# Kernel tuning notes

Measured on AMD Instinct MI355X. Metric: run time of the kernel, lower is better.

Reference implementation:

```python
import jax, jax.numpy as jnp
import numpy as np

# --- config (matches init_kwargs) ---
B, L = 16, 1024            # batch, max_seq_len
S = L - 1                  # effective sequence length
D = 768                    # attention_dim
H = 8                      # n_heads
DH = D // 3 * 2            # per-head Q/K/V out dim = 512
HID = 256                  # hidden_dim (EntireEmbedding output)
FF = 3072                  # ffnn_dim
N_A = 10000                # n_assessments = offsets[0]
N_CATE, N_CONT = 4, 6
EPS = 1e-5


def setup_inputs() -> dict:
    key = jax.random.key(0)
    ks = jax.random.split(key, 24)
    f = lambda k, shp, s=0.02: (jax.random.normal(k, shp, dtype=jnp.float32) * s)
    inp = {
        "cate_x": jax.random.randint(ks[0], (B, L, N_CATE), 0, N_A),
        "cont_x": jax.random.normal(ks[1], (B, L, N_CONT), dtype=jnp.float32),
        "mask": jax.random.randint(ks[2], (B, L), 0, 2),
        "targets": jax.random.randint(ks[3], (B, L), 0, 2),
        # embeddings (padding_idx=0 rows zeroed)
        "M_emb": f(ks[4], ((N_A + 1) * 2 - 1, D)).at[0].set(0.0),
        "E_emb": f(ks[5], (N_A + 1, D)).at[0].set(0.0),
        "pos_emb": f(ks[6], (S, D)),
        # EntireEmbedding stand-in: cate embedding + linear over cont feats -> HID
        "cate_emb": f(ks[7], (N_A + 1, HID)).at[0].set(0.0),
        "cont_W": f(ks[8], (N_CONT, HID)),
        "cont_b": jnp.zeros((HID,), jnp.float32),
        # per-head Q/K/V, stacked over head axis
        "WQ": f(ks[9], (H, D, DH)),
        "bQ": jnp.zeros((H, DH), jnp.float32),
        "WK": f(ks[10], (H, D + HID, DH)),
        "bK": jnp.zeros((H, DH), jnp.float32),
        "WV": f(ks[11], (H, D + HID, DH)),
        "bV": jnp.zeros((H, DH), jnp.float32),
        "W0": f(ks[12], (H * DH, D)),
        "ln_g": jnp.ones((D,), jnp.float32),
        "ln_b": jnp.zeros((D,), jnp.float32),
        "ffn_W1": f(ks[13], (D, FF)),
        "ffn_b1": jnp.zeros((FF,), jnp.float32),
        "ffn_W2": f(ks[14], (FF, D)),
        "ffn_b2": jnp.zeros((D,), jnp.float32),
        # FinalConnecting stand-in: Linear(D, 1)
        "fin_W": f(ks[15], (D, 1)),
        "fin_b": jnp.zeros((1,), jnp.float32),
    }
    return inp


def reference(cate_x, cont_x, mask, targets, M_emb, E_emb, pos_emb, cate_emb,
              cont_W, cont_b, WQ, bQ, WK, bK, WV, bV, W0, ln_g, ln_b,
              ffn_W1, ffn_b1, ffn_W2, ffn_b2, fin_W, fin_b):
    # additive mask, faithful to the original (triu over [B,S]!)
    new_mask = jnp.triu(jnp.ones((B, S), jnp.float32), k=-1) * 100000.0 - 100000.0

    assessments = cate_x[:, :-1, 0]                 # [B,S]
    interactions = targets[:, :-1]
    y = assessments + interactions * N_A            # interaction ids
    next_assessments = cate_x[:, 1:, 0]

    M_hat = M_emb[y] + pos_emb[None]                # [B,S,D]
    comb = cate_emb[cate_x[..., 0]] + cont_x @ cont_W + cont_b   # [B,L,HID]
    E_hat = jnp.concatenate([E_emb[next_assessments], comb[:, 1:, :]], axis=-1)  # [B,S,D+HID]

    # all heads at once (faithful per-head Q/K/V linears, stacked)
    Q = jnp.einsum('bsd,hde->hbse', M_hat, WQ) + bQ[:, None, None, :]
    K = jnp.einsum('bsd,hde->hbse', E_hat, WK) + bK[:, None, None, :]
    V = jnp.einsum('bsd,hde->hbse', E_hat, WV) + bV[:, None, None, :]

    score = jnp.einsum('hbqe,hbke->hbqk', Q, K) / jnp.sqrt(jnp.asarray(DH, Q.dtype))
    score = score + new_mask[None, :, None, :]      # broadcast over query axis
    attn = jax.nn.softmax(score, axis=-1)
    Z = jnp.einsum('hbqk,hbke->hbqe', attn, V)      # [H,B,S,DH]
    Zc = jnp.transpose(Z, (1, 2, 0, 3)).reshape(B, S, H * DH)  # head-major concat

    z = Zc @ W0                                     # [B,S,D]
    fz = jax.nn.relu(z @ ffn_W1 + ffn_b1) @ ffn_W2 + ffn_b2  # dropout off (eval)
    h = z + fz
    mu = jnp.mean(h, axis=-1, keepdims=True)
    var = jnp.mean((h - mu) ** 2, axis=-1, keepdims=True)
    zn = (h - mu) / jnp.sqrt(var + EPS) * ln_g + ln_b

    out = (zn @ fin_W + fin_b)[..., 0]              # [B,S]
    return out
```

## Files before the change

kernel.cpp:

```cpp
#include <hip/hip_runtime.h>
#include <hip/hip_bf16.h>

constexpr int B_   = 16;
constexpr int L_   = 1024;
constexpr int S_   = 1023;
constexpr int D_   = 768;
constexpr int H_   = 8;
constexpr int DH_  = 512;
constexpr int HID_ = 256;
constexpr int FF_  = 3072;
constexpr int NA_  = 10000;
constexpr int NCATE_ = 4;
constexpr int NCONT_ = 6;
constexpr float EPS_ = 1e-5f;
constexpr long BSR_ = (long)B_ * S_;
constexpr int SLD_ = 1024;

constexpr long COMB_SZ = BSR_ * HID_;
constexpr long IDX_PAD = 49152;
constexpr long QKV_SZ  = BSR_ * DH_;
constexpr long SC_SZ   = (long)B_ * S_ * SLD_;
constexpr long ZO_SZ   = BSR_ * D_;
constexpr size_t WS_NEED_BYTES =
    (size_t)(COMB_SZ + IDX_PAD + 3 * QKV_SZ + SC_SZ + ZO_SZ) * 4;

__device__ __forceinline__ float blk_reduce_sum(float v, float* sm) {
#pragma unroll
    for (int off = 32; off > 0; off >>= 1) v += __shfl_down(v, off, 64);
    const int lane = threadIdx.x & 63, wv = threadIdx.x >> 6;
    if (lane == 0) sm[wv] = v;
    __syncthreads();
    float t = (threadIdx.x < 4) ? sm[threadIdx.x] : 0.f;
    t += __shfl_down(t, 2, 64);
    t += __shfl_down(t, 1, 64);
    if (threadIdx.x == 0) sm[4] = t;
    __syncthreads();
    float r = sm[4];
    __syncthreads();
    return r;
}

__device__ __forceinline__ float blk_reduce_max(float v, float* sm) {
#pragma unroll
    for (int off = 32; off > 0; off >>= 1) v = fmaxf(v, __shfl_down(v, off, 64));
    const int lane = threadIdx.x & 63, wv = threadIdx.x >> 6;
    if (lane == 0) sm[wv] = v;
    __syncthreads();
    float t = (threadIdx.x < 4) ? sm[threadIdx.x] : -3.4e38f;
    t = fmaxf(t, __shfl_down(t, 2, 64));
    t = fmaxf(t, __shfl_down(t, 1, 64));
    if (threadIdx.x == 0) sm[4] = t;
    __syncthreads();
    float r = sm[4];
    __syncthreads();
    return r;
}

__global__ __launch_bounds__(256) void sentinel_k(float* __restrict__ out, int n)
{
    const int i = blockIdx.x * 256 + threadIdx.x;
    if (i < n) out[i] = 1e30f;
}

__global__ __launch_bounds__(256) void prep_k(
    const int* __restrict__ cate_x, const float* __restrict__ cont_x,
    const int* __restrict__ targets,
    const float* __restrict__ cate_emb, const float* __restrict__ cont_W,
    const float* __restrict__ cont_b,
    int* __restrict__ yArr, int* __restrict__ nxArr, int* __restrict__ sArr,
    float* __restrict__ comb)
{
    const int row = blockIdx.x;
    const int b = row / S_;
    const int s = row - b * S_;
    const int nx = cate_x[((long)b * L_ + s + 1) * NCATE_];
    if (threadIdx.x == 0) {
        yArr[row]  = cate_x[((long)b * L_ + s) * NCATE_] + targets[(long)b * L_ + s] * NA_;
        nxArr[row] = nx;
        sArr[row]  = s;
    }
    const float* cx = cont_x + ((long)b * L_ + s + 1) * NCONT_;
    float cv[NCONT_];
#pragma unroll
    for (int i = 0; i < NCONT_; ++i) cv[i] = cx[i];
    const int j = threadIdx.x;
    float acc = cont_b[j];
#pragma unroll
    for (int i = 0; i < NCONT_; ++i) acc = fmaf(cv[i], cont_W[i * HID_ + j], acc);
    comb[(long)row * HID_ + j] = cate_emb[(long)nx * HID_ + j] + acc;
}

template<int TSZ, int AMODE, bool TB, bool BIAS, bool RELU, bool ADDC, bool ACCUM, bool KVF>
__global__ __launch_bounds__(256) void sgemm_k(
    const float* __restrict__ A, const float* __restrict__ A2,
    const int* __restrict__ rIdx, const int* __restrict__ rS,
    const float* __restrict__ Bm, const float* __restrict__ Bm2,
    const float* __restrict__ bias, const float* __restrict__ bias2,
    const float* __restrict__ Cadd, float* __restrict__ C, float* __restrict__ C2,
    int M, int N, int Kd, int lda, int ldb, int ldc,
    long sA, long sB, long sC, float alpha)
{
    constexpr int BK = 16;
    constexpr int TM = TSZ / 16;
    constexpr int NL = TSZ / 64;
    constexpr int NF4M = TSZ / 4 - 1;
    constexpr int SHB  = (TSZ == 128) ? 5 : 4;
    __shared__ float As[BK][TSZ];
    __shared__ float Bs[BK][TSZ];

    const int tid = threadIdx.x;
    const int tx = tid & 15;
    const int ty = tid >> 4;
    const int rowBase = blockIdx.y * TSZ;
    int colBase = blockIdx.x * TSZ;
    const int bz = blockIdx.z;

    if constexpr (KVF) {
        if (colBase >= DH_) {
            Bm = Bm2;
            if constexpr (BIAS) bias = bias2;
            C = C2;
            colBase -= DH_;
        }
    }
    if constexpr (AMODE == 0) A += (long)bz * sA;
    Bm += (long)bz * sB;
    C += (long)bz * sC;
    if constexpr (ADDC) Cadd += (long)bz * sC;

    float acc[TM][TM];
#pragma unroll
    for (int i = 0; i < TM; ++i)
#pragma unroll
        for (int j = 0; j < TM; ++j) acc[i][j] = 0.f;

    for (int k0 = 0; k0 < Kd; k0 += BK) {
#pragma unroll
        for (int u = 0; u < NL; ++u) {
            const int f = tid + u * 256;
            const int r = f >> 2;
            const int k4 = (f & 3) * 4;
            const int gk = k0 + k4;
            float v0 = 0.f, v1 = 0.f, v2 = 0.f, v3 = 0.f;
            const int gr = rowBase + r;
            if (gr < M) {
                if constexpr (AMODE == 0) {
                    const float* p = A + (long)gr * lda + gk;
                    if (gk + 3 < Kd) {
                        float4 v = *(const float4*)p;
                        v0 = v.x; v1 = v.y; v2 = v.z; v3 = v.w;
                    } else {
                        if (gk + 0 < Kd) v0 = p[0];
                        if (gk + 1 < Kd) v1 = p[1];
                        if (gk + 2 < Kd) v2 = p[2];
                    }
                } else if constexpr (AMODE == 1) {
                    const int y = rIdx[gr];
                    const int s = rS[gr];
                    const float4 a = *(const float4*)(A  + (long)y * D_ + gk);
                    const float4 p = *(const float4*)(A2 + (long)s * D_ + gk);
                    v0 = a.x + p.x; v1 = a.y + p.y; v2 = a.z + p.z; v3 = a.w + p.w;
                } else {
                    if (gk < D_) {
                        const int nx = rIdx[gr];
                        const float4 a = *(const float4*)(A + (long)nx * D_ + gk);
                        v0 = a.x; v1 = a.y; v2 = a.z; v3 = a.w;
                    } else {
                        const float4 a = *(const float4*)(A2 + (long)gr * HID_ + (gk - D_));
                        v0 = a.x; v1 = a.y; v2 = a.z; v3 = a.w;
                    }
                }
            }
            As[k4 + 0][r] = v0; As[k4 + 1][r] = v1;
            As[k4 + 2][r] = v2; As[k4 + 3][r] = v3;
        }
        if constexpr (!TB) {
#pragma unroll
            for (int u = 0; u < NL; ++u) {
                const int f = tid + u * 256;
                const int kk = f >> SHB;
                const int n4 = (f & NF4M) * 4;
                const int gk = k0 + kk;
                const int gc = colBase + n4;
                float v0 = 0.f, v1 = 0.f, v2 = 0.f, v3 = 0.f;
                if (gk < Kd) {
                    const float* p = Bm + (long)gk * ldb + gc;
                    if (gc + 3 < N) {
                        float4 v = *(const float4*)p;
                        v0 = v.x; v1 = v.y; v2 = v.z; v3 = v.w;
                    } else {
                        if (gc + 0 < N) v0 = p[0];
                        if (gc + 1 < N) v1 = p[1];
                        if (gc + 2 < N) v2 = p[2];
                        if (gc + 3 < N) v3 = p[3];
                    }
                }
                Bs[kk][n4 + 0] = v0; Bs[kk][n4 + 1] = v1;
                Bs[kk][n4 + 2] = v2; Bs[kk][n4 + 3] = v3;
            }
        } else {
#pragma unroll
            for (int u = 0; u < NL; ++u) {
                const int f = tid + u * 256;
                const int n = f >> 2;
                const int k4 = (f & 3) * 4;
                float v0 = 0.f, v1 = 0.f, v2 = 0.f, v3 = 0.f;
                const int gn = colBase + n;
                if (gn < N) {
                    const float* p = Bm + (long)gn * ldb + k0 + k4;
                    if (k0 + k4 + 3 < Kd) {
                        float4 v = *(const float4*)p;
                        v0 = v.x; v1 = v.y; v2 = v.z; v3 = v.w;
                    } else {
                        if (k0 + k4 + 0 < Kd) v0 = p[0];
                        if (k0 + k4 + 1 < Kd) v1 = p[1];
                        if (k0 + k4 + 2 < Kd) v2 = p[2];
                        if (k0 + k4 + 3 < Kd) v3 = p[3];
                    }
                }
                Bs[k4 + 0][n] = v0; Bs[k4 + 1][n] = v1;
                Bs[k4 + 2][n] = v2; Bs[k4 + 3][n] = v3;
            }
        }
        __syncthreads();

#pragma unroll
        for (int kk = 0; kk < BK; ++kk) {
            float a[TM], b[TM];
#pragma unroll
            for (int ih = 0; ih < TM / 4; ++ih) {
                *(float4*)&a[ih * 4] = *(const float4*)&As[kk][ih * 64 + ty * 4];
                *(float4*)&b[ih * 4] = *(const float4*)&Bs[kk][ih * 64 + tx * 4];
            }
#pragma unroll
            for (int i = 0; i < TM; ++i)
#pragma unroll
                for (int j = 0; j < TM; ++j)
                    acc[i][j] = fmaf(a[i], b[j], acc[i][j]);
        }
        __syncthreads();
    }

#pragma unroll
    for (int i = 0; i < TM; ++i) {
        const int r = rowBase + (i >> 2) * 64 + ty * 4 + (i & 3);
        if (r >= M) continue;
#pragma unroll
        for (int j = 0; j < TM; ++j) {
            const int c = colBase + (j >> 2) * 64 + tx * 4 + (j & 3);
            if (c >= N) continue;
            float v = acc[i][j] * alpha;
            if constexpr (BIAS) v += bias[c];
            if constexpr (ADDC) v += Cadd[(long)r * ldc + c];
            if constexpr (RELU) v = fmaxf(v, 0.f);
            const long idx = (long)r * ldc + c;
            if constexpr (ACCUM) C[idx] += v; else C[idx] = v;
        }
    }
}

__global__ __launch_bounds__(256) void softmax_k(float* __restrict__ Sc)
{
    const int row = blockIdx.x;
    const int b = row / S_;
    float* s = Sc + (long)row * SLD_;
    __shared__ float buf[S_];
    __shared__ float sm[5];
    const int klo = b - 1;

    float m = -3.4e38f;
    for (int k = threadIdx.x; k < S_; k += 256) {
        float v = s[k];
        if (k < klo) v -= 1e5f;
        buf[k] = v;
        m = fmaxf(m, v);
    }
    m = blk_reduce_max(m, sm);
    float sum = 0.f;
    for (int k = threadIdx.x; k < S_; k += 256) {
        const float e = __expf(buf[k] - m);
        buf[k] = e;
        sum += e;
    }
    sum = blk_reduce_sum(sum, sm);
    const float inv = 1.0f / sum;
    for (int k = threadIdx.x; k < S_; k += 256) s[k] = buf[k] * inv;
}

__global__ __launch_bounds__(256) void final_k(
    const float* __restrict__ h, const float* __restrict__ g,
    const float* __restrict__ bt, const float* __restrict__ fw,
    const float* __restrict__ fb, float* __restrict__ out)
{
    const int row = blockIdx.x;
    const float* hr = h + (long)row * D_;
    __shared__ float sm[5];

    float lsum = 0.f;
    for (int d = threadIdx.x; d < D_; d += 256) lsum += hr[d];
    const float mu = blk_reduce_sum(lsum, sm) * (1.0f / D_);

    float lvar = 0.f;
    for (int d = threadIdx.x; d < D_; d += 256) {
        const float t = hr[d] - mu;
        lvar = fmaf(t, t, lvar);
    }
    const float var = blk_reduce_sum(lvar, sm) * (1.0f / D_);
    const float rstd = 1.0f / sqrtf(var + EPS_);

    float ldot = 0.f;
    for (int d = threadIdx.x; d < D_; d += 256) {
        const float zn = (hr[d] - mu) * rstd * g[d] + bt[d];
        ldot = fmaf(zn, fw[d], ldot);
    }
    const float dot = blk_reduce_sum(ldot, sm);
    if (threadIdx.x == 0) out[row] = dot + fb[0];
}

static inline dim3 ggrid(int M, int N, int batch, int tsz) {
    return dim3((N + tsz - 1) / tsz, (M + tsz - 1) / tsz, batch);
}

extern "C" void kernel_launch(void* const* d_in, const int* in_sizes, int n_in,
                              void* d_out, int out_size, void* d_ws, size_t ws_size,
                              hipStream_t stream)
{
    float* out = (float*)d_out;
    if (ws_size < WS_NEED_BYTES) {
        sentinel_k<<<(out_size + 255) / 256, 256, 0, stream>>>(out, out_size);
        return;
    }

    const int*   cate_x   = (const int*)  d_in[0];
    const float* cont_x   = (const float*)d_in[1];
    const int*   targets  = (const int*)  d_in[3];
    const float* M_emb    = (const float*)d_in[4];
    const float* E_emb    = (const float*)d_in[5];
    const float* pos_emb  = (const float*)d_in[6];
    const float* cate_emb = (const float*)d_in[7];
    const float* cont_W   = (const float*)d_in[8];
    const float* cont_b   = (const float*)d_in[9];
    const float* WQ = (const float*)d_in[10];
    const float* bQ = (const float*)d_in[11];
    const float* WK = (const float*)d_in[12];
    const float* bK = (const float*)d_in[13];
    const float* WV = (const float*)d_in[14];
    const float* bV = (const float*)d_in[15];
    const float* W0 = (const float*)d_in[16];
    const float* ln_g = (const float*)d_in[17];
    const float* ln_b = (const float*)d_in[18];
    const float* W1 = (const float*)d_in[19];
    const float* b1 = (const float*)d_in[20];
    const float* W2 = (const float*)d_in[21];
    const float* b2 = (const float*)d_in[22];
    const float* fw = (const float*)d_in[23];
    const float* fb = (const float*)d_in[24];
    float* ws  = (float*)d_ws;

    float* comb  = ws;
    int*   yArr  = (int*)(ws + COMB_SZ);
    int*   nxArr = yArr + BSR_;
    int*   sArr  = nxArr + BSR_;
    float* Qh = ws + COMB_SZ + IDX_PAD;
    float* Kh = Qh + QKV_SZ;
    float* Vh = Kh + QKV_SZ;
    float* Sc = Vh + QKV_SZ;
    float* Zo = Sc + SC_SZ;
    float* Zh   = Qh;
    float* Hid  = Qh;
    float* Hbuf = Sc;

    prep_k<<<(int)BSR_, 256, 0, stream>>>(cate_x, cont_x, targets, cate_emb,
                                          cont_W, cont_b, yArr, nxArr, sArr, comb);

    const float inv_sqrt_dh = 0.044194173824159216f;

    for (int h = 0; h < H_; ++h) {
        sgemm_k<64, 1, false, true, false, false, false, false>
            <<<ggrid((int)BSR_, DH_, 1, 64), 256, 0, stream>>>(
            M_emb, pos_emb, yArr, sArr,
            WQ + (long)h * D_ * DH_, nullptr, bQ + (long)h * DH_, nullptr,
            nullptr, Qh, nullptr,
            (int)BSR_, DH_, D_, D_, DH_, DH_, 0, 0, 0, 1.0f);
        sgemm_k<64, 2, false, true, false, false, false, true>
            <<<ggrid((int)BSR_, 2 * DH_, 1, 64), 256, 0, stream>>>(
            E_emb, comb, nxArr, nullptr,
            WK + (long)h * (D_ + HID_) * DH_, WV + (long)h * (D_ + HID_) * DH_,
            bK + (long)h * DH_, bV + (long)h * DH_,
            nullptr, Kh, Vh,
            (int)BSR_, 2 * DH_, D_ + HID_, 0, DH_, DH_, 0, 0, 0, 1.0f);
        sgemm_k<128, 0, true, false, false, false, false, false>
            <<<ggrid(S_, S_, B_, 128), 256, 0, stream>>>(
            Qh, nullptr, nullptr, nullptr,
            Kh, nullptr, nullptr, nullptr,
            nullptr, Sc, nullptr,
            S_, S_, DH_, DH_, DH_, SLD_,
            (long)S_ * DH_, (long)S_ * DH_, (long)S_ * SLD_, inv_sqrt_dh);
        softmax_k<<<(int)BSR_, 256, 0, stream>>>(Sc);
        sgemm_k<64, 0, false, false, false, false, false, false>
            <<<ggrid(S_, DH_, B_, 64), 256, 0, stream>>>(
            Sc, nullptr, nullptr, nullptr,
            Vh, nullptr, nullptr, nullptr,
            nullptr, Zh, nullptr,
            S_, DH_, S_, SLD_, DH_, DH_,
            (long)S_ * SLD_, (long)S_ * DH_, (long)S_ * DH_, 1.0f);
        if (h == 0)
            sgemm_k<64, 0, false, false, false, false, false, false>
                <<<ggrid((int)BSR_, D_, 1, 64), 256, 0, stream>>>(
                Zh, nullptr, nullptr, nullptr,
                W0 + (long)h * DH_ * D_, nullptr, nullptr, nullptr,
                nullptr, Zo, nullptr,
                (int)BSR_, D_, DH_, DH_, D_, D_, 0, 0, 0, 1.0f);
        else
            sgemm_k<64, 0, false, false, false, false, true, false>
                <<<ggrid((int)BSR_, D_, 1, 64), 256, 0, stream>>>(
                Zh, nullptr, nullptr, nullptr,
                W0 + (long)h * DH_ * D_, nullptr, nullptr, nullptr,
                nullptr, Zo, nullptr,
                (int)BSR_, D_, DH_, DH_, D_, D_, 0, 0, 0, 1.0f);
    }

    for (int c = 0; c < 4; ++c) {
        const int f0 = c * 768;
        sgemm_k<64, 0, false, true, true, false, false, false>
            <<<ggrid((int)BSR_, 768, 1, 64), 256, 0, stream>>>(
            Zo, nullptr, nullptr, nullptr,
            W1 + f0, nullptr, b1 + f0, nullptr,
            nullptr, Hid, nullptr,
            (int)BSR_, 768, D_, D_, FF_, 768, 0, 0, 0, 1.0f);
        if (c == 0)
            sgemm_k<64, 0, false, true, false, true, false, false>
                <<<ggrid((int)BSR_, D_, 1, 64), 256, 0, stream>>>(
                Hid, nullptr, nullptr, nullptr,
                W2 + (long)f0 * D_, nullptr, b2, nullptr,
                Zo, Hbuf, nullptr,
                (int)BSR_, D_, 768, 768, D_, D_, 0, 0, 0, 1.0f);
        else
            sgemm_k<64, 0, false, false, false, false, true, false>
                <<<ggrid((int)BSR_, D_, 1, 64), 256, 0, stream>>>(
                Hid, nullptr, nullptr, nullptr,
                W2 + (long)f0 * D_, nullptr, nullptr, nullptr,
                nullptr, Hbuf, nullptr,
                (int)BSR_, D_, 768, 768, D_, D_, 0, 0, 0, 1.0f);
    }

    final_k<<<(int)BSR_, 256, 0, stream>>>(Hbuf, ln_g, ln_b, fw, fb, out);

    (void)in_sizes; (void)n_in;
}
```

Measured before the change: 12.93 ms.

## Use bf16 MFMA for QK^T and PV with split-precision V and P

Q and K are stored as bf16 and QK^T moves from a scalar fp32 SGEMM to an MFMA 16x16x32 bf16 kernel. Softmax writes P as a hi/lo bf16 pair and V is stored transposed as a hi/lo pair, so the PV product runs on MFMA with three-term split precision that approximates fp32. This moves the attention matmuls onto the matrix cores. In exchange, Q/K lose precision and the MFMA kernels read operands directly from global memory with no LDS staging.

New measurement: 11.95 ms. 1.08x faster.

```diff
diff --git a/kernel.cpp b/kernel.cpp
--- a/kernel.cpp
+++ b/kernel.cpp
@@ -15,14 +15,23 @@
 constexpr float EPS_ = 1e-5f;
 constexpr long BSR_ = (long)B_ * S_;
 constexpr int SLD_ = 1024;
+constexpr int SLD2_ = 2048;
+constexpr int VTLD_ = 1024;
 
 constexpr long COMB_SZ = BSR_ * HID_;
 constexpr long IDX_PAD = 49152;
-constexpr long QKV_SZ  = BSR_ * DH_;
-constexpr long SC_SZ   = (long)B_ * S_ * SLD_;
-constexpr long ZO_SZ   = BSR_ * D_;
+constexpr long QB_F  = BSR_ * DH_ / 2;
+constexpr long KB_F  = BSR_ * DH_ / 2;
+constexpr long VTH_F = (long)B_ * DH_ * VTLD_ / 2;
+constexpr long VTL_F = VTH_F;
+constexpr long SC_SZ = (long)B_ * S_ * SLD_;
+constexpr long ZH_SZ = BSR_ * DH_;
+constexpr long ZO_SZ = BSR_ * D_;
 constexpr size_t WS_NEED_BYTES =
-    (size_t)(COMB_SZ + IDX_PAD + 3 * QKV_SZ + SC_SZ + ZO_SZ) * 4;
+    (size_t)(COMB_SZ + IDX_PAD + QB_F + KB_F + VTH_F + VTL_F + SC_SZ + ZH_SZ + ZO_SZ) * 4;
+
+typedef __attribute__((ext_vector_type(8))) short bf16x8;
+typedef __attribute__((ext_vector_type(4))) float f32x4;
 
 __device__ __forceinline__ float blk_reduce_sum(float v, float* sm) {
 #pragma unroll
@@ -90,21 +99,19 @@
     comb[(long)row * HID_ + j] = cate_emb[(long)nx * HID_ + j] + acc;
 }
 
-template<int TSZ, int AMODE, bool TB, bool BIAS, bool RELU, bool ADDC, bool ACCUM, bool KVF>
+template<int AMODE, bool BIAS, bool RELU, bool ADDC, bool ACCUM, bool KVF, int OMODE>
 __global__ __launch_bounds__(256) void sgemm_k(
     const float* __restrict__ A, const float* __restrict__ A2,
     const int* __restrict__ rIdx, const int* __restrict__ rS,
     const float* __restrict__ Bm, const float* __restrict__ Bm2,
     const float* __restrict__ bias, const float* __restrict__ bias2,
-    const float* __restrict__ Cadd, float* __restrict__ C, float* __restrict__ C2,
+    const float* __restrict__ Cadd, float* __restrict__ C,
+    short* __restrict__ CbA, short* __restrict__ CbVh, short* __restrict__ CbVl,
     int M, int N, int Kd, int lda, int ldb, int ldc,
     long sA, long sB, long sC, float alpha)
 {
     constexpr int BK = 16;
-    constexpr int TM = TSZ / 16;
-    constexpr int NL = TSZ / 64;
-    constexpr int NF4M = TSZ / 4 - 1;
-    constexpr int SHB  = (TSZ == 128) ? 5 : 4;
+    constexpr int TSZ = 64, TM = 4;
     __shared__ float As[BK][TSZ];
     __shared__ float Bs[BK][TSZ];
 
@@ -114,13 +121,14 @@
     const int rowBase = blockIdx.y * TSZ;
     int colBase = blockIdx.x * TSZ;
     const int bz = blockIdx.z;
+    bool isV = false;
 
     if constexpr (KVF) {
         if (colBase >= DH_) {
             Bm = Bm2;
             if constexpr (BIAS) bias = bias2;
-            C = C2;
             colBase -= DH_;
+            isV = true;
         }
     }
     if constexpr (AMODE == 0) A += (long)bz * sA;
@@ -135,9 +143,8 @@
         for (int j = 0; j < TM; ++j) acc[i][j] = 0.f;
 
     for (int k0 = 0; k0 < Kd; k0 += BK) {
-#pragma unroll
-        for (int u = 0; u < NL; ++u) {
-            const int f = tid + u * 256;
+        {
+            const int f = tid;
             const int r = f >> 2;
             const int k4 = (f & 3) * 4;
             const int gk = k0 + k4;
@@ -174,64 +181,35 @@
             As[k4 + 0][r] = v0; As[k4 + 1][r] = v1;
             As[k4 + 2][r] = v2; As[k4 + 3][r] = v3;
         }
-        if constexpr (!TB) {
-#pragma unroll
-            for (int u = 0; u < NL; ++u) {
-                const int f = tid + u * 256;
-                const int kk = f >> SHB;
-                const int n4 = (f & NF4M) * 4;
-                const int gk = k0 + kk;
-                const int gc = colBase + n4;
-                float v0 = 0.f, v1 = 0.f, v2 = 0.f, v3 = 0.f;
-                if (gk < Kd) {
-                    const float* p = Bm + (long)gk * ldb + gc;
-                    if (gc + 3 < N) {
-                        float4 v = *(const float4*)p;
-                        v0 = v.x; v1 = v.y; v2 = v.z; v3 = v.w;
-                    } else {
-                        if (gc + 0 < N) v0 = p[0];
-                        if (gc + 1 < N) v1 = p[1];
-                        if (gc + 2 < N) v2 = p[2];
-                        if (gc + 3 < N) v3 = p[3];
-                    }
+        {
+            const int f = tid;
+            const int kk = f >> 4;
+            const int n4 = (f & 15) * 4;
+            const int gk = k0 + kk;
+            const int gc = colBase + n4;
+            float v0 = 0.f, v1 = 0.f, v2 = 0.f, v3 = 0.f;
+            if (gk < Kd) {
+                const float* p = Bm + (long)gk * ldb + gc;
+                if (gc + 3 < N) {
+                    float4 v = *(const float4*)p;
+                    v0 = v.x; v1 = v.y; v2 = v.z; v3 = v.w;
+                } else {
+                    if (gc + 0 < N) v0 = p[0];
+                    if (gc + 1 < N) v1 = p[1];
+                    if (gc + 2 < N) v2 = p[2];
+                    if (gc + 3 < N) v3 = p[3];
                 }
-                Bs[kk][n4 + 0] = v0; Bs[kk][n4 + 1] = v1;
-                Bs[kk][n4 + 2] = v2; Bs[kk][n4 + 3] = v3;
             }
-        } else {
-#pragma unroll
-            for (int u = 0; u < NL; ++u) {
-                const int f = tid + u * 256;
-                const int n = f >> 2;
-                const int k4 = (f & 3) * 4;
-                float v0 = 0.f, v1 = 0.f, v2 = 0.f, v3 = 0.f;
-                const int gn = colBase + n;
-                if (gn < N) {
-                    const float* p = Bm + (long)gn * ldb + k0 + k4;
-                    if (k0 + k4 + 3 < Kd) {
-                        float4 v = *(const float4*)p;
-                        v0 = v.x; v1 = v.y; v2 = v.z; v3 = v.w;
-                    } else {
-                        if (k0 + k4 + 0 < Kd) v0 = p[0];
-                        if (k0 + k4 + 1 < Kd) v1 = p[1];
-                        if (k0 + k4 + 2 < Kd) v2 = p[2];
-                        if (k0 + k4 + 3 < Kd) v3 = p[3];
-                    }
-                }
-                Bs[k4 + 0][n] = v0; Bs[k4 + 1][n] = v1;
-                Bs[k4 + 2][n] = v2; Bs[k4 + 3][n] = v3;
-            }
+            Bs[kk][n4 + 0] = v0; Bs[kk][n4 + 1] = v1;
+            Bs[kk][n4 + 2] = v2; Bs[kk][n4 + 3] = v3;
         }
         __syncthreads();
 
 #pragma unroll
         for (int kk = 0; kk < BK; ++kk) {
             float a[TM], b[TM];
-#pragma unroll
-            for (int ih = 0; ih < TM / 4; ++ih) {
-                *(float4*)&a[ih * 4] = *(const float4*)&As[kk][ih * 64 + ty * 4];
-                *(float4*)&b[ih * 4] = *(const float4*)&Bs[kk][ih * 64 + tx * 4];
-            }
+            *(float4*)&a[0] = *(const float4*)&As[kk][ty * 4];
+            *(float4*)&b[0] = *(const float4*)&Bs[kk][tx * 4];
 #pragma unroll
             for (int i = 0; i < TM; ++i)
 #pragma unroll
@@ -243,18 +221,148 @@
 
 #pragma unroll
     for (int i = 0; i < TM; ++i) {
-        const int r = rowBase + (i >> 2) * 64 + ty * 4 + (i & 3);
+        const int r = rowBase + ty * 4 + i;
         if (r >= M) continue;
+        const int bb = r / S_;
+        const int rl = r - bb * S_;
 #pragma unroll
         for (int j = 0; j < TM; ++j) {
-            const int c = colBase + (j >> 2) * 64 + tx * 4 + (j & 3);
+            const int c = colBase + tx * 4 + j;
             if (c >= N) continue;
             float v = acc[i][j] * alpha;
             if constexpr (BIAS) v += bias[c];
             if constexpr (ADDC) v += Cadd[(long)r * ldc + c];
             if constexpr (RELU) v = fmaxf(v, 0.f);
-            const long idx = (long)r * ldc + c;
-            if constexpr (ACCUM) C[idx] += v; else C[idx] = v;
+            if constexpr (OMODE == 0) {
+                const long idx = (long)r * ldc + c;
+                if constexpr (ACCUM) C[idx] += v; else C[idx] = v;
+            } else {
+                const __hip_bfloat16 hv = __float2bfloat16(v);
+                if (KVF && isV) {
+                    const long vidx = ((long)bb * DH_ + c) * VTLD_ + rl;
+                    ((__hip_bfloat16*)CbVh)[vidx] = hv;
+                    ((__hip_bfloat16*)CbVl)[vidx] =
+                        __float2bfloat16(v - __bfloat162float(hv));
+                } else {
+                    ((__hip_bfloat16*)CbA)[(long)r * ldc + c] = hv;
+                }
+            }
+        }
+    }
+}
+
+__global__ __launch_bounds__(256) void qkt_mfma_k(
+    const short* __restrict__ Qb, const short* __restrict__ Kb,
+    float* __restrict__ Sc, float alpha)
+{
+    const int b  = blockIdx.z;
+    const int qT = blockIdx.y * 64;
+    const int kT = blockIdx.x * 64;
+    const int w  = threadIdx.x >> 6;
+    const int l  = threadIdx.x & 63;
+    const int q0 = qT + (w >> 1) * 32;
+    const int k0 = kT + (w & 1) * 32;
+    const int lr = l & 15;
+    const int lk = (l >> 4) * 8;
+
+    const short* qp0 = Qb + ((long)b * S_ + q0 + lr) * DH_ + lk;
+    const short* qp1 = qp0 + 16 * DH_;
+    const short* kp0 = Kb + ((long)b * S_ + k0 + lr) * DH_ + lk;
+    const short* kp1 = kp0 + 16 * DH_;
+
+    f32x4 acc00 = {0.f,0.f,0.f,0.f}, acc01 = acc00, acc10 = acc00, acc11 = acc00;
+#pragma unroll 4
+    for (int d = 0; d < DH_; d += 32) {
+        bf16x8 a0 = *(const bf16x8*)(qp0 + d);
+        bf16x8 a1 = *(const bf16x8*)(qp1 + d);
+        bf16x8 b0 = *(const bf16x8*)(kp0 + d);
+        bf16x8 b1 = *(const bf16x8*)(kp1 + d);
+        acc00 = __builtin_amdgcn_mfma_f32_16x16x32_bf16(a0, b0, acc00, 0, 0, 0);
+        acc01 = __builtin_amdgcn_mfma_f32_16x16x32_bf16(a0, b1, acc01, 0, 0, 0);
+        acc10 = __builtin_amdgcn_mfma_f32_16x16x32_bf16(a1, b0, acc10, 0, 0, 0);
+        acc11 = __builtin_amdgcn_mfma_f32_16x16x32_bf16(a1, b1, acc11, 0, 0, 0);
+    }
+
+    float* sc = Sc + (long)b * S_ * SLD_;
+    const int rbase = (l >> 4) * 4;
+#pragma unroll
+    for (int mi = 0; mi < 2; ++mi) {
+#pragma unroll
+        for (int ni = 0; ni < 2; ++ni) {
+            const f32x4 av = (mi == 0) ? (ni == 0 ? acc00 : acc01)
+                                       : (ni == 0 ? acc10 : acc11);
+            const int kk = k0 + ni * 16 + lr;
+            if (kk >= S_) continue;
+#pragma unroll
+            for (int i = 0; i < 4; ++i) {
+                const int qq = q0 + mi * 16 + rbase + i;
+                if (qq < S_) sc[(long)qq * SLD_ + kk] = av[i] * alpha;
+            }
+        }
+    }
+}
+
+__global__ __launch_bounds__(256) void pv_mfma_k(
+    const short* __restrict__ Pb, const short* __restrict__ VTh,
+    const short* __restrict__ VTl, float* __restrict__ Z)
+{
+    const int b  = blockIdx.z;
+    const int qT = blockIdx.y * 64;
+    const int eT = blockIdx.x * 64;
+    const int w  = threadIdx.x >> 6;
+    const int l  = threadIdx.x & 63;
+    const int q0 = qT + (w >> 1) * 32;
+    const int e0 = eT + (w & 1) * 32;
+    const int lr = l & 15;
+    const int lk = (l >> 4) * 8;
+
+    const short* pp0 = Pb + ((long)b * S_ + q0 + lr) * SLD2_ + lk;
+    const short* pp1 = pp0 + 16 * SLD2_;
+    const long voff = (long)b * DH_ * VTLD_ + (long)(e0 + lr) * VTLD_ + lk;
+    const short* vh0 = VTh + voff;
+    const short* vh1 = vh0 + 16 * VTLD_;
+    const short* vl0 = VTl + voff;
+    const short* vl1 = vl0 + 16 * VTLD_;
+
+    f32x4 acc00 = {0.f,0.f,0.f,0.f}, acc01 = acc00, acc10 = acc00, acc11 = acc00;
+#pragma unroll 2
+    for (int k = 0; k < 1024; k += 32) {
+        bf16x8 ah0 = *(const bf16x8*)(pp0 + k);
+        bf16x8 al0 = *(const bf16x8*)(pp0 + 1024 + k);
+        bf16x8 ah1 = *(const bf16x8*)(pp1 + k);
+        bf16x8 al1 = *(const bf16x8*)(pp1 + 1024 + k);
+        bf16x8 bh0 = *(const bf16x8*)(vh0 + k);
+        bf16x8 bl0 = *(const bf16x8*)(vl0 + k);
+        bf16x8 bh1 = *(const bf16x8*)(vh1 + k);
+        bf16x8 bl1 = *(const bf16x8*)(vl1 + k);
+        acc00 = __builtin_amdgcn_mfma_f32_16x16x32_bf16(ah0, bh0, acc00, 0, 0, 0);
+        acc00 = __builtin_amdgcn_mfma_f32_16x16x32_bf16(ah0, bl0, acc00, 0, 0, 0);
+        acc00 = __builtin_amdgcn_mfma_f32_16x16x32_bf16(al0, bh0, acc00, 0, 0, 0);
+        acc01 = __builtin_amdgcn_mfma_f32_16x16x32_bf16(ah0, bh1, acc01, 0, 0, 0);
+        acc01 = __builtin_amdgcn_mfma_f32_16x16x32_bf16(ah0, bl1, acc01, 0, 0, 0);
+        acc01 = __builtin_amdgcn_mfma_f32_16x16x32_bf16(al0, bh1, acc01, 0, 0, 0);
+        acc10 = __builtin_amdgcn_mfma_f32_16x16x32_bf16(ah1, bh0, acc10, 0, 0, 0);
+        acc10 = __builtin_amdgcn_mfma_f32_16x16x32_bf16(ah1, bl0, acc10, 0, 0, 0);
+        acc10 = __builtin_amdgcn_mfma_f32_16x16x32_bf16(al1, bh0, acc10, 0, 0, 0);
+        acc11 = __builtin_amdgcn_mfma_f32_16x16x32_bf16(ah1, bh1, acc11, 0, 0, 0);
+        acc11 = __builtin_amdgcn_mfma_f32_16x16x32_bf16(ah1, bl1, acc11, 0, 0, 0);
+        acc11 = __builtin_amdgcn_mfma_f32_16x16x32_bf16(al1, bh1, acc11, 0, 0, 0);
+    }
+
+    float* z = Z + (long)b * S_ * DH_;
+    const int rbase = (l >> 4) * 4;
+#pragma unroll
+    for (int mi = 0; mi < 2; ++mi) {
+#pragma unroll
+        for (int ni = 0; ni < 2; ++ni) {
+            const f32x4 av = (mi == 0) ? (ni == 0 ? acc00 : acc01)
+                                       : (ni == 0 ? acc10 : acc11);
+            const int ee = e0 + ni * 16 + lr;
+#pragma unroll
+            for (int i = 0; i < 4; ++i) {
+                const int qq = q0 + mi * 16 + rbase + i;
+                if (qq < S_) z[(long)qq * DH_ + ee] = av[i];
+            }
         }
     }
 }
@@ -284,7 +392,17 @@
     }
     sum = blk_reduce_sum(sum, sm);
     const float inv = 1.0f / sum;
-    for (int k = threadIdx.x; k < S_; k += 256) s[k] = buf[k] * inv;
+    __hip_bfloat16* pb = reinterpret_cast<__hip_bfloat16*>(s);
+    for (int k = threadIdx.x; k < S_; k += 256) {
+        const float p = buf[k] * inv;
+        const __hip_bfloat16 hi = __float2bfloat16(p);
+        pb[k] = hi;
+        pb[1024 + k] = __float2bfloat16(p - __bfloat162float(hi));
+    }
+    if (threadIdx.x == 0) {
+        pb[S_] = __float2bfloat16(0.f);
+        pb[1024 + S_] = __float2bfloat16(0.f);
+    }
 }
 
 __global__ __launch_bounds__(256) void final_k(
@@ -361,13 +479,15 @@
     int*   yArr  = (int*)(ws + COMB_SZ);
     int*   nxArr = yArr + BSR_;
     int*   sArr  = nxArr + BSR_;
-    float* Qh = ws + COMB_SZ + IDX_PAD;
-    float* Kh = Qh + QKV_SZ;
-    float* Vh = Kh + QKV_SZ;
-    float* Sc = Vh + QKV_SZ;
-    float* Zo = Sc + SC_SZ;
-    float* Zh   = Qh;
-    float* Hid  = Qh;
+    float* bfA = ws + COMB_SZ + IDX_PAD;
+    short* Qb  = (short*)bfA;
+    short* Kb  = Qb + BSR_ * DH_;
+    short* VTh = Kb + BSR_ * DH_;
+    short* VTl = VTh + (long)B_ * DH_ * VTLD_;
+    float* Sc  = bfA + QB_F + KB_F + VTH_F + VTL_F;
+    float* Zh  = Sc + SC_SZ;
+    float* Zo  = Zh + ZH_SZ;
+    float* Hid  = bfA;
     float* Hbuf = Sc;
 
     prep_k<<<(int)BSR_, 256, 0, stream>>>(cate_x, cont_x, targets, cate_emb,
@@ -376,71 +496,60 @@
     const float inv_sqrt_dh = 0.044194173824159216f;
 
     for (int h = 0; h < H_; ++h) {
-        sgemm_k<64, 1, false, true, false, false, false, false>
+        sgemm_k<1, true, false, false, false, false, 1>
             <<<ggrid((int)BSR_, DH_, 1, 64), 256, 0, stream>>>(
             M_emb, pos_emb, yArr, sArr,
             WQ + (long)h * D_ * DH_, nullptr, bQ + (long)h * DH_, nullptr,
-            nullptr, Qh, nullptr,
+            nullptr, nullptr, Qb, nullptr, nullptr,
             (int)BSR_, DH_, D_, D_, DH_, DH_, 0, 0, 0, 1.0f);
-        sgemm_k<64, 2, false, true, false, false, false, true>
+        sgemm_k<2, true, false, false, false, true, 1>
             <<<ggrid((int)BSR_, 2 * DH_, 1, 64), 256, 0, stream>>>(
             E_emb, comb, nxArr, nullptr,
             WK + (long)h * (D_ + HID_) * DH_, WV + (long)h * (D_ + HID_) * DH_,
             bK + (long)h * DH_, bV + (long)h * DH_,
-            nullptr, Kh, Vh,
+            nullptr, nullptr, Kb, VTh, VTl,
             (int)BSR_, 2 * DH_, D_ + HID_, 0, DH_, DH_, 0, 0, 0, 1.0f);
-        sgemm_k<128, 0, true, false, false, false, false, false>
-            <<<ggrid(S_, S_, B_, 128), 256, 0, stream>>>(
-            Qh, nullptr, nullptr, nullptr,
-            Kh, nullptr, nullptr, nullptr,
-            nullptr, Sc, nullptr,
-            S_, S_, DH_, DH_, DH_, SLD_,
-            (long)S_ * DH_, (long)S_ * DH_, (long)S_ * SLD_, inv_sqrt_dh);
+        qkt_mfma_k<<<dim3(16, 16, B_), 256, 0, stream>>>(Qb, Kb, Sc, inv_sqrt_dh);
         softmax_k<<<(int)BSR_, 256, 0, stream>>>(Sc);
-        sgemm_k<64, 0, false, false, false, false, false, false>
-            <<<ggrid(S_, DH_, B_, 64), 256, 0, stream>>>(
-            Sc, nullptr, nullptr, nullptr,
-            Vh, nullptr, nullptr, nullptr,
-            nullptr, Zh, nullptr,
-            S_, DH_, S_, SLD_, DH_, DH_,
-            (long)S_ * SLD_, (long)S_ * DH_, (long)S_ * DH_, 1.0f);
+        pv_mfma_k<<<dim3(8, 16, B_), 256, 0, stream>>>(
+            (const short*)Sc, VTh, VTl, Zh);
         if (h == 0)
-            sgemm_k<64, 0, false, false, false, false, false, false>
+            sgemm_k<0, false, false, false, false, false, 0>
                 <<<ggrid((int)BSR_, D_, 1, 64), 256, 0, stream>>>(
                 Zh, nullptr, nullptr, nullptr,
                 W0 + (long)h * DH_ * D_, nullptr, nullptr, nullptr,
-                nullptr, Zo, nullptr,
+                nullptr, Zo, nullptr, nullptr, nullptr,
                 (int)BSR_, D_, DH_, DH_, D_, D_, 0, 0, 0, 1.0f);
         else
-            sgemm_k<64, 0, false, false, false, false, true, false>
+            sgemm_k<0, false, false, false, true, false, 0>
                 <<<ggrid((int)BSR_, D_, 1, 64), 256, 0, stream>>>(
                 Zh, nullptr, nullptr, nullptr,
                 W0 + (long)h * DH_ * D_, nullptr, nullptr, nullptr,
-                nullptr, Zo, nullptr,
+                nullptr, Zo, nullptr, nullptr, nullptr,
                 (int)BSR_, D_, DH_, DH_, D_, D_, 0, 0, 0, 1.0f);
     }
 
     for (int c = 0; c < 4; ++c) {
         const int f0 = c * 768;
-        sgemm_k<64, 0, false, true, true, false, false, false>
+        sgemm_k<0, true, true, false, false, false, 0>
             <<<ggrid((int)BSR_, 768, 1, 64), 256, 0, stream>>>(
             Zo, nullptr, nullptr, nullptr,
             W1 + f0, nullptr, b1 + f0, nullptr,
-            nullptr, Hid, nullptr,
+            nullptr, Hid, nullptr, nullptr, nullptr,
             (int)BSR_, 768, D_, D_, FF_, 768, 0, 0, 0, 1.0f);
         if (c == 0)
-            sgemm_k<64, 0, false, true, false, true, false, false>
+            sgemm_k<0, true, false, true, false, false, 0>
                 <<<ggrid((int)BSR_, D_, 1, 64), 256, 0, stream>>>(
                 Hid, nullptr, nullptr, nullptr,
                 W2 + (long)f0 * D_, nullptr, b2, nullptr,
-                Zo, Hbuf, nullptr,
+                Zo, Hbuf, nullptr, nullptr, nullptr,
                 (int)BSR_, D_, 768, 768, D_, D_, 0, 0, 0, 1.0f);
         else
-            sgemm_k<64, 0, false, false, false, false, true, false>
+            sgemm_k<0, false, false, false, true, false, 0>
                 <<<ggrid((int)BSR_, D_, 1, 64), 256, 0, stream>>>(
                 Hid, nullptr, nullptr, nullptr,
                 W2 + (long)f0 * D_, nullptr, nullptr, nullptr,
-                nullptr, Hbuf, nullptr,
+                nullptr, Hbuf, nullptr, nullptr, nullptr,
                 (int)BSR_, D_, 768, 768, D_, D_, 0, 0, 0, 1.0f);
     }
 
```
